# Performance work log

Hardware: AMD Instinct MI355X
Metric: run time of the kernel (lower is better)

The kernel has to match this reference:

```python
import jax, jax.numpy as jnp
import numpy as np

HIDDEN = 4096
N_HEADS = 32
N_KV_HEADS = 8
HEAD_DIM = HIDDEN // N_HEADS  # 128
INTER = 11008
EPS = 1e-6
ROPE_THETA = 10000.0
B, S = 2, 2048


def setup_inputs() -> dict:
    key = jax.random.key(0)
    ks = jax.random.split(key, 8)
    sc = 0.02
    return {
        "hidden_states": jax.random.normal(ks[0], (B, S, HIDDEN), dtype=jnp.float32),
        "positions": jnp.arange(S, dtype=jnp.int32),
        "w_qkv": jax.random.normal(ks[1], (HIDDEN, (N_HEADS + 2 * N_KV_HEADS) * HEAD_DIM), dtype=jnp.float32) * sc,
        "w_o": jax.random.normal(ks[2], (N_HEADS * HEAD_DIM, HIDDEN), dtype=jnp.float32) * sc,
        "w_gate_up": jax.random.normal(ks[3], (HIDDEN, 2 * INTER), dtype=jnp.float32) * sc,
        "w_down": jax.random.normal(ks[4], (INTER, HIDDEN), dtype=jnp.float32) * sc,
        "ln1_w": jnp.ones((HIDDEN,), dtype=jnp.float32),
        "ln2_w": jnp.ones((HIDDEN,), dtype=jnp.float32),
    }


def _rms_norm(x, w):
    var = jnp.mean(jnp.square(x), axis=-1, keepdims=True)
    return x * jax.lax.rsqrt(var + EPS) * w


def _rope(x, positions):
    # x: [B, S, H, D]; NeoX-style rotary over full head_dim
    d = x.shape[-1]
    inv_freq = 1.0 / (ROPE_THETA ** (jnp.arange(0, d, 2, dtype=jnp.float32) / d))
    freqs = positions.astype(jnp.float32)[:, None] * inv_freq[None, :]  # [S, D/2]
    cos = jnp.cos(freqs)[None, :, None, :]
    sin = jnp.sin(freqs)[None, :, None, :]
    x1, x2 = jnp.split(x, 2, axis=-1)
    return jnp.concatenate([x1 * cos - x2 * sin, x2 * cos + x1 * sin], axis=-1)


def _decoder_layer(hidden_states, positions, w_qkv, w_o, w_gate_up, w_down, ln1_w, ln2_w):
    b, s, _ = hidden_states.shape
    scale = HEAD_DIM ** -0.5

    # --- attention block ---
    residual = hidden_states
    x = _rms_norm(hidden_states, ln1_w)
    qkv = x @ w_qkv
    q, k, v = jnp.split(qkv, [N_HEADS * HEAD_DIM, (N_HEADS + N_KV_HEADS) * HEAD_DIM], axis=-1)
    q = q.reshape(b, s, N_HEADS, HEAD_DIM)
    k = k.reshape(b, s, N_KV_HEADS, HEAD_DIM)
    v = v.reshape(b, s, N_KV_HEADS, HEAD_DIM)
    q = _rope(q, positions)
    k = _rope(k, positions)
    # GQA: expand kv heads
    g = N_HEADS // N_KV_HEADS
    k = jnp.repeat(k, g, axis=2)  # [B, S, H, D]
    v = jnp.repeat(v, g, axis=2)
    scores = jnp.einsum("bqhd,bkhd->bhqk", q, k) * scale
    causal = jnp.tril(jnp.ones((s, s), dtype=bool))
    scores = jnp.where(causal[None, None], scores, jnp.finfo(scores.dtype).min)
    probs = jax.nn.softmax(scores, axis=-1)
    attn = jnp.einsum("bhqk,bkhd->bqhd", probs, v).reshape(b, s, N_HEADS * HEAD_DIM)
    hidden_states = residual + attn @ w_o

    # --- MLP block (SwiGLU) ---
    residual = hidden_states
    x = _rms_norm(hidden_states, ln2_w)
    gate_up = x @ w_gate_up
    gate, up = jnp.split(gate_up, 2, axis=-1)
    hidden_states = residual + (jax.nn.silu(gate) * up) @ w_down
    return hidden_states


def reference(hidden_states, positions, w_qkv, w_o, w_gate_up, w_down, ln1_w, ln2_w):
    return _decoder_layer(hidden_states, positions, w_qkv, w_o, w_gate_up, w_down, ln1_w, ln2_w)
```

## Files before the change

kernel.cpp:

```cpp
#include <hip/hip_runtime.h>


typedef __attribute__((ext_vector_type(8))) short bf16x8;
typedef __attribute__((ext_vector_type(4))) float f32x4;

__device__ __forceinline__ ushort f2bf(float f) {
  unsigned u = __float_as_uint(f);
  return (ushort)((u + 0x7fffu + ((u >> 16) & 1u)) >> 16);
}
__device__ __forceinline__ float bf2f(ushort u) {
  union { unsigned u32; float f; } x; x.u32 = ((unsigned)u) << 16; return x.f;
}
__device__ __forceinline__ void gload16(const void* g, void* l) {
  __builtin_amdgcn_global_load_lds((__attribute__((address_space(1))) void*)g,
                                   (__attribute__((address_space(3))) void*)l,
                                   16, 0, 0);
}

#define BARRIER() asm volatile("s_barrier" ::: "memory")
#define WAIT_LGKM0() asm volatile("s_waitcnt lgkmcnt(0)" ::: "memory")
#define WAIT_VM8() asm volatile("s_waitcnt vmcnt(8)" ::: "memory")
#define WAIT_VM4() asm volatile("s_waitcnt vmcnt(4)" ::: "memory")
#define WAIT_VM0() asm volatile("s_waitcnt vmcnt(0)" ::: "memory")

__global__ __launch_bounds__(256) void rmsnorm_kernel(
    const float* __restrict__ x, const float* __restrict__ g,
    ushort* __restrict__ out) {
  const int row = blockIdx.x, t = threadIdx.x;
  const float4* xp = (const float4*)(x + (size_t)row * 4096);
  float4 v[4]; float ss = 0.f;
#pragma unroll
  for (int i = 0; i < 4; ++i) {
    v[i] = xp[t + i * 256];
    ss += v[i].x * v[i].x + v[i].y * v[i].y + v[i].z * v[i].z + v[i].w * v[i].w;
  }
#pragma unroll
  for (int m = 32; m; m >>= 1) ss += __shfl_xor(ss, m);
  __shared__ float red[4];
  if ((t & 63) == 0) red[t >> 6] = ss;
  __syncthreads();
  float inv = rsqrtf((red[0] + red[1] + red[2] + red[3]) * (1.f / 4096.f) + 1e-6f);
  const float4* gp = (const float4*)g;
  ushort* op = out + (size_t)row * 4096;
#pragma unroll
  for (int i = 0; i < 4; ++i) {
    float4 gv = gp[t + i * 256];
    ushort4 o;
    o.x = f2bf(v[i].x * inv * gv.x); o.y = f2bf(v[i].y * inv * gv.y);
    o.z = f2bf(v[i].z * inv * gv.z); o.w = f2bf(v[i].w * inv * gv.w);
    *(ushort4*)(op + (size_t)(t + i * 256) * 4) = o;
  }
}

__global__ __launch_bounds__(256) void transpose_cast_kernel(
    const float* __restrict__ in, ushort* __restrict__ out,
    int ld_in, int col_off, int R) {
  __shared__ ushort tile[64][68];
  const int t = threadIdx.x;
  const int r0 = blockIdx.x * 64, c0 = blockIdx.y * 64;
  const int rl = t >> 2, cl = (t & 3) * 16;
  const float* ip = in + (size_t)(r0 + rl) * ld_in + col_off + c0 + cl;
#pragma unroll
  for (int i = 0; i < 4; ++i) {
    float4 f = ((const float4*)ip)[i];
    tile[rl][cl + i * 4 + 0] = f2bf(f.x);
    tile[rl][cl + i * 4 + 1] = f2bf(f.y);
    tile[rl][cl + i * 4 + 2] = f2bf(f.z);
    tile[rl][cl + i * 4 + 3] = f2bf(f.w);
  }
  __syncthreads();
  union { ushort us[8]; uint4 v; } pk0, pk1;
#pragma unroll
  for (int j = 0; j < 8; ++j) pk0.us[j] = tile[cl + j][rl];
#pragma unroll
  for (int j = 0; j < 8; ++j) pk1.us[j] = tile[cl + 8 + j][rl];
  uint4* op = (uint4*)(out + (size_t)(c0 + rl) * R + r0 + cl);
  op[0] = pk0.v; op[1] = pk1.v;
}

template <typename OutT, bool RES>
__global__ __launch_bounds__(512, 2) void gemm256_kernel(
    const ushort* __restrict__ A, const ushort* __restrict__ Bt,
    OutT* __restrict__ C, const float* __restrict__ res,
    int M, int N, int K) {
  extern __shared__ ushort lds[];
  ushort* Al = lds;
  ushort* Bl = lds + 32768;
  const int t = threadIdx.x, l = t & 63, w = t >> 6;
  const int wr = w >> 2, wc = w & 3;
  const int lr = l & 15, lg = l >> 4;
  const int rhi = lr >> 3, rlo = lr & 7;
  const int srow = l >> 3, sg = (l & 7) ^ srow;

  const int nbx = N >> 8;
  const int nwg = nbx * (M >> 8);
  const int cpx = nwg >> 3;
  const int bid = (int)blockIdx.x;
  const int swz = (bid & 7) * cpx + (bid >> 3);
  const int n0 = (swz % nbx) << 8, m0 = (swz / nbx) << 8;

  const int lof0 = rhi * 512 + rlo * 64 + ((0 + lg) ^ rlo) * 8;
  const int lof1 = rhi * 512 + rlo * 64 + ((4 + lg) ^ rlo) * 8;

  const f32x4 fz = {0.f, 0.f, 0.f, 0.f};
  f32x4 acc[8][4];
#pragma unroll
  for (int i = 0; i < 8; ++i)
#pragma unroll
    for (int j = 0; j < 4; ++j) acc[i][j] = fz;
  bf16x8 a[8][2];
  bf16x8 bq[2][2];

  const ushort* Asrc = A + (size_t)(m0 + w * 8 + srow) * K + sg * 8;
  const ushort* Bsrc = Bt + (size_t)(n0 + w * 8 + srow) * K + sg * 8;
  const size_t rK64 = (size_t)64 * K, rK128 = (size_t)128 * K;
  ushort* Adst = Al + w * 512;
  ushort* Bdst = Bl + w * 512;

#define STAGE_A(buf, half, tile) do {                                   \
    const ushort* s_ = Asrc + (size_t)(half) * rK128 + ((tile) << 6);   \
    ushort* d_ = Adst + (buf) * 16384 + (half) * 8192;                  \
    gload16(s_, d_);                                                    \
    gload16(s_ + rK64, d_ + 4096);                                      \
  } while (0)
#define STAGE_B(buf, half, tile) do {                                   \
    const ushort* s_ = Bsrc + (size_t)(half) * rK128 + ((tile) << 6);   \
    ushort* d_ = Bdst + (buf) * 16384 + (half) * 8192;                  \
    gload16(s_, d_);                                                    \
    gload16(s_ + rK64, d_ + 4096);                                      \
  } while (0)
#define LDA4(AH, QM) do {                                                   \
    _Pragma("unroll") for (int mi_ = 0; mi_ < 4; ++mi_) {                   \
      a[(QM) * 4 + mi_][0] =                                                \
          *(const bf16x8*)((AH) + ((QM) * 4 + mi_) * 1024 + lof0);          \
      a[(QM) * 4 + mi_][1] =                                                \
          *(const bf16x8*)((AH) + ((QM) * 4 + mi_) * 1024 + lof1);          \
    } } while (0)
#define LDB2(BH, NQ) do {                                                   \
    _Pragma("unroll") for (int nj_ = 0; nj_ < 2; ++nj_) {                   \
      bq[nj_][0] = *(const bf16x8*)((BH) + ((NQ) * 2 + nj_) * 1024 + lof0); \
      bq[nj_][1] = *(const bf16x8*)((BH) + ((NQ) * 2 + nj_) * 1024 + lof1); \
    } } while (0)
#define MFMA16(QM, QN)                                                      \
    __builtin_amdgcn_s_setprio(1);                                          \
    _Pragma("unroll") for (int mi_ = 0; mi_ < 4; ++mi_)                     \
    _Pragma("unroll") for (int nj_ = 0; nj_ < 2; ++nj_) {                   \
      acc[(QM) * 4 + mi_][(QN) * 2 + nj_] =                                 \
          __builtin_amdgcn_mfma_f32_16x16x32_bf16(                          \
              a[(QM) * 4 + mi_][0], bq[nj_][0],                             \
              acc[(QM) * 4 + mi_][(QN) * 2 + nj_], 0, 0, 0);                \
      acc[(QM) * 4 + mi_][(QN) * 2 + nj_] =                                 \
          __builtin_amdgcn_mfma_f32_16x16x32_bf16(                          \
              a[(QM) * 4 + mi_][1], bq[nj_][1],                             \
              acc[(QM) * 4 + mi_][(QN) * 2 + nj_], 0, 0, 0);                \
    }                                                                       \
    __builtin_amdgcn_s_setprio(0);

  const ushort* A0h = Al + wr * 8192;
  const ushort* A1h = A0h + 16384;
  const ushort* B0h = Bl + (wc >> 1) * 8192 + (wc & 1) * 4096;
  const ushort* B1h = B0h + 16384;

  const int ntiles = K >> 6, nIter = K >> 7;
  STAGE_A(0, 0, 0); STAGE_A(0, 1, 0); STAGE_B(0, 0, 0); STAGE_B(0, 1, 0);
  STAGE_A(1, 0, 1); STAGE_A(1, 1, 1);
  WAIT_VM4(); BARRIER();

  for (int it = 0; it < nIter; ++it) {
    const int u = it * 2;
    LDA4(A0h, 0); LDB2(B0h, 0);
    STAGE_B(1, 0, u + 1);
    BARRIER(); WAIT_LGKM0(); MFMA16(0, 0); BARRIER();
    LDA4(A0h, 1);
    STAGE_B(1, 1, u + 1);
    BARRIER(); WAIT_LGKM0(); MFMA16(1, 0); BARRIER();
    LDB2(B0h, 1);
    if (u + 2 < ntiles) STAGE_A(0, 0, u + 2);
    BARRIER(); WAIT_LGKM0(); MFMA16(0, 1); BARRIER();
    if (u + 2 < ntiles) STAGE_A(0, 1, u + 2);
    BARRIER(); MFMA16(1, 1);
    if (u + 2 < ntiles) { WAIT_VM4(); } else { WAIT_VM0(); }
    BARRIER();
    LDA4(A1h, 0); LDB2(B1h, 0);
    if (u + 2 < ntiles) STAGE_B(0, 0, u + 2);
    BARRIER(); WAIT_LGKM0(); MFMA16(0, 0); BARRIER();
    LDA4(A1h, 1);
    if (u + 2 < ntiles) STAGE_B(0, 1, u + 2);
    BARRIER(); WAIT_LGKM0(); MFMA16(1, 0); BARRIER();
    LDB2(B1h, 1);
    if (u + 3 < ntiles) STAGE_A(1, 0, u + 3);
    BARRIER(); WAIT_LGKM0(); MFMA16(0, 1); BARRIER();
    if (u + 3 < ntiles) STAGE_A(1, 1, u + 3);
    BARRIER(); MFMA16(1, 1);
    WAIT_VM4(); BARRIER();
  }

#pragma unroll
  for (int mi = 0; mi < 8; ++mi)
#pragma unroll
    for (int ni = 0; ni < 4; ++ni)
#pragma unroll
      for (int r = 0; r < 4; ++r) {
        int row = m0 + wr * 128 + mi * 16 + lg * 4 + r;
        int col = n0 + wc * 64 + ni * 16 + lr;
        size_t idx = (size_t)row * N + col;
        float v = acc[mi][ni][r];
        if (RES) v += res[idx];
        if constexpr (sizeof(OutT) == 2) C[idx] = f2bf(v);
        else                             C[idx] = v;
      }
#undef STAGE_A
#undef STAGE_B
#undef LDA4
#undef LDB2
#undef MFMA16
}

__global__ void rope_table_kernel(const int* __restrict__ pos,
                                  float2* __restrict__ tab) {
  int idx = blockIdx.x * 256 + threadIdx.x;
  int s = idx >> 6, fi = idx & 63;
  float inv = (float)exp(-(double)(2 * fi) / 128.0 * 9.210340371976184);
  float a = (float)pos[s] * inv;
  tab[idx] = make_float2(cosf(a), sinf(a));
}

__global__ __launch_bounds__(256) void rope_scatter_kernel(
    const ushort* __restrict__ qkv, const float2* __restrict__ tab,
    ushort* __restrict__ Qr, ushort* __restrict__ Kr, ushort* __restrict__ Vt) {
  __shared__ ushort vt[64][132];
  const int t = threadIdx.x, tt = blockIdx.x, h = blockIdx.y;
  const int row = t >> 2, c = (t & 3) * 16;
  const int tok = tt * 64 + row;
  const int b = tok >> 11, s = tok & 2047;
  const ushort* ip = qkv + (size_t)tok * 6144 + h * 128;
  union U { uint4 v; ushort us[8]; };
  U a0, a1, b0, b1;
  a0.v = *(const uint4*)(ip + c);      a1.v = *(const uint4*)(ip + c + 8);
  b0.v = *(const uint4*)(ip + c + 64); b1.v = *(const uint4*)(ip + c + 72);
  if (h < 40) {
    U o0, o1, o2, o3;
#pragma unroll
    for (int j = 0; j < 8; ++j) {
      float2 cs = tab[s * 64 + c + j];
      float x1 = bf2f(a0.us[j]), x2 = bf2f(b0.us[j]);
      o0.us[j] = f2bf(x1 * cs.x - x2 * cs.y);
      o2.us[j] = f2bf(x2 * cs.x + x1 * cs.y);
    }
#pragma unroll
    for (int j = 0; j < 8; ++j) {
      float2 cs = tab[s * 64 + c + 8 + j];
      float x1 = bf2f(a1.us[j]), x2 = bf2f(b1.us[j]);
      o1.us[j] = f2bf(x1 * cs.x - x2 * cs.y);
      o3.us[j] = f2bf(x2 * cs.x + x1 * cs.y);
    }
    ushort* base;
    if (h < 32) base = Qr + ((size_t)((b * 32 + h) * 2048 + s)) * 128;
    else        base = Kr + ((size_t)((b * 8 + (h - 32)) * 2048 + s)) * 128;
    *(uint4*)(base + c)      = o0.v; *(uint4*)(base + c + 8)  = o1.v;
    *(uint4*)(base + c + 64) = o2.v; *(uint4*)(base + c + 72) = o3.v;
  } else {
    const int hv = h - 40;
#pragma unroll
    for (int j = 0; j < 8; ++j) {
      vt[row][c + j]      = a0.us[j]; vt[row][c + 8 + j]  = a1.us[j];
      vt[row][c + 64 + j] = b0.us[j]; vt[row][c + 72 + j] = b1.us[j];
    }
    __syncthreads();
    const int d = t >> 1, s0 = (t & 1) * 32, sb = (tt & 31) * 64;
    U w0, w1, w2, w3;
#pragma unroll
    for (int j = 0; j < 8; ++j) {
      w0.us[j] = vt[s0 + j][d];      w1.us[j] = vt[s0 + 8 + j][d];
      w2.us[j] = vt[s0 + 16 + j][d]; w3.us[j] = vt[s0 + 24 + j][d];
    }
    ushort* vb = Vt + ((size_t)((b * 8 + hv) * 128 + d)) * 2048 + sb + s0;
    *(uint4*)(vb) = w0.v;      *(uint4*)(vb + 8) = w1.v;
    *(uint4*)(vb + 16) = w2.v; *(uint4*)(vb + 24) = w3.v;
  }
}

__global__ __launch_bounds__(256) void attn_kernel(
    const ushort* __restrict__ Q, const ushort* __restrict__ K,
    const ushort* __restrict__ V, ushort* __restrict__ O) {
  extern __shared__ ushort sm[];
  ushort* Kl = sm;
  ushort* Vl = sm + 16384;
  ushort* Pl = sm + 32768;
  const int t = threadIdx.x, l = t & 63, w = t >> 6;
  const int lr = l & 15, lg = l >> 4;
  const int qt = blockIdx.x, h = blockIdx.y, b = blockIdx.z;
  const int hkv = h >> 2;
  const f32x4 fzero = {0.f, 0.f, 0.f, 0.f};

  const int rm = lr & 7;
  int ksw[4], vsw[2];
#pragma unroll
  for (int ks = 0; ks < 4; ++ks) ksw[ks] = ((ks * 4 + lg) ^ rm) * 8;
  vsw[0] = (lg ^ rm) * 8;
  vsw[1] = ((4 + lg) ^ rm) * 8;
  const int kcol = ((t & 15) ^ ((t >> 4) & 7)) * 8;
  const int vcol = ((t & 7) ^ ((t >> 3) & 7)) * 8;

  const ushort* qp =
      Q + ((size_t)((b * 32 + h) * 2048 + qt * 64 + w * 16 + lr)) * 128 + lg * 8;
  bf16x8 qf[4];
#pragma unroll
  for (int ks = 0; ks < 4; ++ks) qf[ks] = *(const bf16x8*)(qp + ks * 32);
  WAIT_VM0();

  const ushort* kg = K + ((size_t)(b * 8 + hkv)) * 2048 * 128;
  const ushort* vg = V + ((size_t)(b * 8 + hkv)) * 128 * 2048;

#define STAGE_KV(buf, s0_) do {                                              \
    _Pragma("unroll") for (int i_ = 0; i_ < 4; ++i_)                         \
      gload16(kg + (size_t)((s0_) + i_ * 16 + (t >> 4)) * 128 + kcol,        \
              (char*)Kl + (buf) * 16384 + i_ * 4096 + t * 16);               \
    _Pragma("unroll") for (int i_ = 0; i_ < 4; ++i_)                         \
      gload16(vg + (size_t)(i_ * 32 + (t >> 3)) * 2048 + (s0_) + vcol,       \
              (char*)Vl + (buf) * 16384 + i_ * 4096 + t * 16);               \
  } while (0)

  f32x4 accO[8];
#pragma unroll
  for (int i = 0; i < 8; ++i) accO[i] = fzero;
  float m_r[4] = {-1e30f, -1e30f, -1e30f, -1e30f};
  float l_r[4] = {0.f, 0.f, 0.f, 0.f};
  const float scale = 0.08838834764831845f;
  const int qrow = qt * 64 + w * 16 + lg * 4;

  STAGE_KV(0, 0);
  for (int j = 0; j <= qt; ++j) {
    if (j < qt) { STAGE_KV((j + 1) & 1, (j + 1) * 64); WAIT_VM8(); }
    else        { WAIT_VM0(); }
    BARRIER();
    const ushort* Kb = Kl + (j & 1) * 8192;
    const ushort* Vb = Vl + (j & 1) * 8192;

    f32x4 sc[4];
#pragma unroll
    for (int ni = 0; ni < 4; ++ni) sc[ni] = fzero;
    __builtin_amdgcn_s_setprio(1);
#pragma unroll
    for (int ni = 0; ni < 4; ++ni)
#pragma unroll
      for (int ks = 0; ks < 4; ++ks) {
        bf16x8 kf = *(const bf16x8*)(Kb + (ni * 16 + lr) * 128 + ksw[ks]);
        sc[ni] = __builtin_amdgcn_mfma_f32_16x16x32_bf16(qf[ks], kf, sc[ni], 0, 0, 0);
      }
    __builtin_amdgcn_s_setprio(0);
    if (j == qt) {
#pragma unroll
      for (int ni = 0; ni < 4; ++ni)
#pragma unroll
        for (int r = 0; r < 4; ++r) {
          float v = sc[ni][r] * scale;
          if (j * 64 + ni * 16 + lr > qrow + r) v = -1e30f;
          sc[ni][r] = v;
        }
    } else {
#pragma unroll
      for (int ni = 0; ni < 4; ++ni)
#pragma unroll
        for (int r = 0; r < 4; ++r) sc[ni][r] *= scale;
    }
    float mnew[4], fsc[4], lad[4];
#pragma unroll
    for (int r = 0; r < 4; ++r) {
      float mx = fmaxf(fmaxf(sc[0][r], sc[1][r]), fmaxf(sc[2][r], sc[3][r]));
#pragma unroll
      for (int m = 8; m; m >>= 1) mx = fmaxf(mx, __shfl_xor(mx, m));
      mnew[r] = fmaxf(m_r[r], mx);
      fsc[r] = __expf(m_r[r] - mnew[r]);
      lad[r] = 0.f;
    }
#pragma unroll
    for (int ni = 0; ni < 4; ++ni)
#pragma unroll
      for (int r = 0; r < 4; ++r) {
        float p = __expf(sc[ni][r] - mnew[r]);
        sc[ni][r] = p;
        lad[r] += p;
      }
#pragma unroll
    for (int r = 0; r < 4; ++r) {
#pragma unroll
      for (int m = 8; m; m >>= 1) lad[r] += __shfl_xor(lad[r], m);
      l_r[r] = l_r[r] * fsc[r] + lad[r];
      m_r[r] = mnew[r];
    }
#pragma unroll
    for (int i = 0; i < 8; ++i)
#pragma unroll
      for (int r = 0; r < 4; ++r) accO[i][r] *= fsc[r];
#pragma unroll
    for (int ni = 0; ni < 4; ++ni)
#pragma unroll
      for (int r = 0; r < 4; ++r) {
        int prow = w * 16 + lg * 4 + r;
        int slot = (ni * 2 + (lr >> 3)) ^ (prow & 7);
        Pl[prow * 64 + slot * 8 + rm] = f2bf(sc[ni][r]);
      }
    WAIT_LGKM0();
    __builtin_amdgcn_s_setprio(1);
#pragma unroll
    for (int ks = 0; ks < 2; ++ks) {
      bf16x8 pf = *(const bf16x8*)(Pl + (w * 16 + lr) * 64 + vsw[ks]);
#pragma unroll
      for (int nf = 0; nf < 8; ++nf) {
        bf16x8 vf = *(const bf16x8*)(Vb + (nf * 16 + lr) * 64 + vsw[ks]);
        accO[nf] = __builtin_amdgcn_mfma_f32_16x16x32_bf16(pf, vf, accO[nf], 0, 0, 0);
      }
    }
    __builtin_amdgcn_s_setprio(0);
    BARRIER();
  }
#undef STAGE_KV
#pragma unroll
  for (int nf = 0; nf < 8; ++nf)
#pragma unroll
    for (int r = 0; r < 4; ++r) {
      int q = qt * 64 + w * 16 + lg * 4 + r;
      int d = nf * 16 + lr;
      float v = accO[nf][r] / l_r[r];
      O[((size_t)(b * 2048 + q)) * 4096 + h * 128 + d] = f2bf(v);
    }
}

__global__ void swiglu_kernel(ushort* __restrict__ gate,
                              const ushort* __restrict__ up, int n8) {
  union U { uint4 v; ushort us[8]; };
  for (int i = blockIdx.x * blockDim.x + threadIdx.x; i < n8;
       i += gridDim.x * blockDim.x) {
    U gv, uv, ov;
    gv.v = ((const uint4*)gate)[i];
    uv.v = ((const uint4*)up)[i];
#pragma unroll
    for (int j = 0; j < 8; ++j) {
      float x = bf2f(gv.us[j]);
      float y = bf2f(uv.us[j]);
      ov.us[j] = f2bf(x / (1.f + __expf(-x)) * y);
    }
    ((uint4*)gate)[i] = ov.v;
  }
}

#define OFF_W    ((size_t)0)
#define OFF_H1   ((size_t)90177536)
#define OFF_XN   ((size_t)157286400)
#define OFF_QKV  ((size_t)190840832)
#define OFF_TAB  ((size_t)241172480)
#define OFF_QR   ((size_t)242221056)
#define OFF_KR   ((size_t)275775488)
#define OFF_VT   ((size_t)284164096)
#define OFF_ATTN ((size_t)292552704)
#define OFF_GATE OFF_QKV
#define OFF_UP   ((size_t)326107136)
#define WS_NEED  ((size_t)416284672)

extern "C" void kernel_launch(void* const* d_in, const int* in_sizes, int n_in,
                              void* d_out, int out_size, void* d_ws,
                              size_t ws_size, hipStream_t stream) {
  (void)in_sizes; (void)n_in; (void)out_size;
  if (ws_size < WS_NEED) return;
  const float* hs     = (const float*)d_in[0];
  const int*   pos    = (const int*)d_in[1];
  const float* w_qkv  = (const float*)d_in[2];
  const float* w_o    = (const float*)d_in[3];
  const float* w_gu   = (const float*)d_in[4];
  const float* w_down = (const float*)d_in[5];
  const float* ln1    = (const float*)d_in[6];
  const float* ln2    = (const float*)d_in[7];
  float* out = (float*)d_out;
  char* ws = (char*)d_ws;

  ushort* W    = (ushort*)(ws + OFF_W);
  float*  h1   = (float*)(ws + OFF_H1);
  ushort* xn   = (ushort*)(ws + OFF_XN);
  ushort* qkv  = (ushort*)(ws + OFF_QKV);
  float2* tab  = (float2*)(ws + OFF_TAB);
  ushort* Qr   = (ushort*)(ws + OFF_QR);
  ushort* Kr   = (ushort*)(ws + OFF_KR);
  ushort* Vt   = (ushort*)(ws + OFF_VT);
  ushort* attn = (ushort*)(ws + OFF_ATTN);
  ushort* gate = (ushort*)(ws + OFF_GATE);
  ushort* up   = (ushort*)(ws + OFF_UP);

  auto kb = gemm256_kernel<ushort, false>;
  auto kf = gemm256_kernel<float, true>;
  hipFuncSetAttribute((const void*)kb, hipFuncAttributeMaxDynamicSharedMemorySize, 131072);
  hipFuncSetAttribute((const void*)kf, hipFuncAttributeMaxDynamicSharedMemorySize, 131072);
  hipFuncSetAttribute((const void*)attn_kernel, hipFuncAttributeMaxDynamicSharedMemorySize, 73728);

  rmsnorm_kernel<<<4096, 256, 0, stream>>>(hs, ln1, xn);
  transpose_cast_kernel<<<dim3(64, 96), 256, 0, stream>>>(w_qkv, W, 6144, 0, 4096);
  gemm256_kernel<ushort, false><<<384, 512, 131072, stream>>>(
      xn, W, qkv, nullptr, 4096, 6144, 4096);
  rope_table_kernel<<<512, 256, 0, stream>>>(pos, tab);
  rope_scatter_kernel<<<dim3(64, 48), 256, 0, stream>>>(qkv, tab, Qr, Kr, Vt);
  attn_kernel<<<dim3(32, 32, 2), 256, 73728, stream>>>(Qr, Kr, Vt, attn);
  transpose_cast_kernel<<<dim3(64, 64), 256, 0, stream>>>(w_o, W, 4096, 0, 4096);
  gemm256_kernel<float, true><<<256, 512, 131072, stream>>>(
      attn, W, h1, hs, 4096, 4096, 4096);

  rmsnorm_kernel<<<4096, 256, 0, stream>>>(h1, ln2, xn);
  transpose_cast_kernel<<<dim3(64, 172), 256, 0, stream>>>(w_gu, W, 22016, 0, 4096);
  gemm256_kernel<ushort, false><<<688, 512, 131072, stream>>>(
      xn, W, gate, nullptr, 4096, 11008, 4096);
  transpose_cast_kernel<<<dim3(64, 172), 256, 0, stream>>>(w_gu, W, 22016, 11008, 4096);
  gemm256_kernel<ushort, false><<<688, 512, 131072, stream>>>(
      xn, W, up, nullptr, 4096, 11008, 4096);
  swiglu_kernel<<<2048, 256, 0, stream>>>(gate, up, (4096 * 11008) / 8);
  transpose_cast_kernel<<<dim3(172, 64), 256, 0, stream>>>(w_down, W, 4096, 0, 11008);
  gemm256_kernel<float, true><<<256, 512, 131072, stream>>>(
      gate, W, out, h1, 4096, 4096, 11008);
}
```

Measured before the change: 1.911 ms.

## Fold softmax scale into Q, lazy rescale, MFMA row-sum in flash attention

Pre-multiplies Q by scale*log2(e) so scores feed exp2 directly without a per-element scale multiply. Skips the running-max rescale of the output accumulator unless some row's max grows by more than 8, in the style of FlashAttention-4. Row sums are computed with an extra MFMA against a ones vector instead of shuffle reductions, and the final division becomes a reciprocal multiply. It also changes the transpose tile padding from 68 to 65. Rounding Q to bf16 after scaling and the bf16 rounding of P in the row sum slightly change numerics.

```diff
diff --git a/kernel.cpp b/kernel.cpp
--- a/kernel.cpp
+++ b/kernel.cpp
@@ -55,7 +55,7 @@
 __global__ __launch_bounds__(256) void transpose_cast_kernel(
     const float* __restrict__ in, ushort* __restrict__ out,
     int ld_in, int col_off, int R) {
-  __shared__ ushort tile[64][68];
+  __shared__ ushort tile[64][65];
   const int t = threadIdx.x;
   const int r0 = blockIdx.x * 64, c0 = blockIdx.y * 64;
   const int rl = t >> 2, cl = (t & 3) * 16;
@@ -302,11 +302,20 @@
   const int kcol = ((t & 15) ^ ((t >> 4) & 7)) * 8;
   const int vcol = ((t & 7) ^ ((t >> 3) & 7)) * 8;
 
+  const float qscale = 0.08838834764831845f * 1.4426950408889634f;
   const ushort* qp =
       Q + ((size_t)((b * 32 + h) * 2048 + qt * 64 + w * 16 + lr)) * 128 + lg * 8;
   bf16x8 qf[4];
 #pragma unroll
-  for (int ks = 0; ks < 4; ++ks) qf[ks] = *(const bf16x8*)(qp + ks * 32);
+  for (int ks = 0; ks < 4; ++ks) {
+    bf16x8 raw = *(const bf16x8*)(qp + ks * 32);
+#pragma unroll
+    for (int j = 0; j < 8; ++j)
+      qf[ks][j] = (short)f2bf(bf2f((ushort)raw[j]) * qscale);
+  }
+  bf16x8 ones;
+#pragma unroll
+  for (int j = 0; j < 8; ++j) ones[j] = (short)0x3F80;
   WAIT_VM0();
 
   const ushort* kg = K + ((size_t)(b * 8 + hkv)) * 2048 * 128;
@@ -326,7 +335,6 @@
   for (int i = 0; i < 8; ++i) accO[i] = fzero;
   float m_r[4] = {-1e30f, -1e30f, -1e30f, -1e30f};
   float l_r[4] = {0.f, 0.f, 0.f, 0.f};
-  const float scale = 0.08838834764831845f;
   const int qrow = qt * 64 + w * 16 + lg * 4;
 
   STAGE_KV(0, 0);
@@ -353,55 +361,40 @@
 #pragma unroll
       for (int ni = 0; ni < 4; ++ni)
 #pragma unroll
-        for (int r = 0; r < 4; ++r) {
-          float v = sc[ni][r] * scale;
-          if (j * 64 + ni * 16 + lr > qrow + r) v = -1e30f;
-          sc[ni][r] = v;
-        }
-    } else {
-#pragma unroll
-      for (int ni = 0; ni < 4; ++ni)
-#pragma unroll
-        for (int r = 0; r < 4; ++r) sc[ni][r] *= scale;
-    }
-    float mnew[4], fsc[4], lad[4];
+        for (int r = 0; r < 4; ++r)
+          if (j * 64 + ni * 16 + lr > qrow + r) sc[ni][r] = -1e30f;
+    }
+    float mx[4];
 #pragma unroll
     for (int r = 0; r < 4; ++r) {
-      float mx = fmaxf(fmaxf(sc[0][r], sc[1][r]), fmaxf(sc[2][r], sc[3][r]));
-#pragma unroll
-      for (int m = 8; m; m >>= 1) mx = fmaxf(mx, __shfl_xor(mx, m));
-      mnew[r] = fmaxf(m_r[r], mx);
-      fsc[r] = __expf(m_r[r] - mnew[r]);
-      lad[r] = 0.f;
-    }
-#pragma unroll
-    for (int ni = 0; ni < 4; ++ni)
+      float v = fmaxf(fmaxf(sc[0][r], sc[1][r]), fmaxf(sc[2][r], sc[3][r]));
+#pragma unroll
+      for (int m = 8; m; m >>= 1) v = fmaxf(v, __shfl_xor(v, m));
+      mx[r] = v;
+    }
+    bool ok = mx[0] <= m_r[0] + 8.f && mx[1] <= m_r[1] + 8.f &&
+              mx[2] <= m_r[2] + 8.f && mx[3] <= m_r[3] + 8.f;
+    if (!__all(ok)) {
 #pragma unroll
       for (int r = 0; r < 4; ++r) {
-        float p = __expf(sc[ni][r] - mnew[r]);
-        sc[ni][r] = p;
-        lad[r] += p;
+        float mnew = fmaxf(m_r[r], mx[r]);
+        float fsc = exp2f(m_r[r] - mnew);
+        l_r[r] *= fsc;
+        m_r[r] = mnew;
+#pragma unroll
+        for (int i = 0; i < 8; ++i) accO[i][r] *= fsc;
       }
-#pragma unroll
-    for (int r = 0; r < 4; ++r) {
-#pragma unroll
-      for (int m = 8; m; m >>= 1) lad[r] += __shfl_xor(lad[r], m);
-      l_r[r] = l_r[r] * fsc[r] + lad[r];
-      m_r[r] = mnew[r];
-    }
-#pragma unroll
-    for (int i = 0; i < 8; ++i)
-#pragma unroll
-      for (int r = 0; r < 4; ++r) accO[i][r] *= fsc[r];
+    }
 #pragma unroll
     for (int ni = 0; ni < 4; ++ni)
 #pragma unroll
       for (int r = 0; r < 4; ++r) {
         int prow = w * 16 + lg * 4 + r;
         int slot = (ni * 2 + (lr >> 3)) ^ (prow & 7);
-        Pl[prow * 64 + slot * 8 + rm] = f2bf(sc[ni][r]);
+        Pl[prow * 64 + slot * 8 + rm] = f2bf(exp2f(sc[ni][r] - m_r[r]));
       }
     WAIT_LGKM0();
+    f32x4 accL = fzero;
     __builtin_amdgcn_s_setprio(1);
 #pragma unroll
     for (int ks = 0; ks < 2; ++ks) {
@@ -411,19 +404,24 @@
         bf16x8 vf = *(const bf16x8*)(Vb + (nf * 16 + lr) * 64 + vsw[ks]);
         accO[nf] = __builtin_amdgcn_mfma_f32_16x16x32_bf16(pf, vf, accO[nf], 0, 0, 0);
       }
+      accL = __builtin_amdgcn_mfma_f32_16x16x32_bf16(pf, ones, accL, 0, 0, 0);
     }
     __builtin_amdgcn_s_setprio(0);
+#pragma unroll
+    for (int r = 0; r < 4; ++r) l_r[r] += accL[r];
     BARRIER();
   }
 #undef STAGE_KV
+  float invl[4];
+#pragma unroll
+  for (int r = 0; r < 4; ++r) invl[r] = 1.f / l_r[r];
 #pragma unroll
   for (int nf = 0; nf < 8; ++nf)
 #pragma unroll
     for (int r = 0; r < 4; ++r) {
       int q = qt * 64 + w * 16 + lg * 4 + r;
       int d = nf * 16 + lr;
-      float v = accO[nf][r] / l_r[r];
-      O[((size_t)(b * 2048 + q)) * 4096 + h * 128 + d] = f2bf(v);
+      O[((size_t)(b * 2048 + q)) * 4096 + h * 128 + d] = f2bf(accO[nf][r] * invl[r]);
     }
 }
 
```

Result: no change. 1.883 ms (-1.5%).
